# Optimization experiments

Measured on AMD Instinct MI355X. Metric: run time of the kernel, lower is better.

## Reference

```python
import jax, jax.numpy as jnp
import numpy as np

NUM_HEADS = 8
HEAD_DIM = 64
EMBED = NUM_HEADS * HEAD_DIM  # 512
KERNEL = 4
TOP_K = 8
SCALING = HEAD_DIM ** (-0.5)


def setup_inputs() -> dict:
    key = jax.random.key(0)
    ks = jax.random.split(key, 5)
    b, s = 4, 4096
    hidden_states = jax.random.normal(ks[0], (b, s, EMBED), dtype=jnp.float32)
    init = 1.0 / np.sqrt(EMBED)
    Wq = jax.random.normal(ks[1], (EMBED, EMBED), dtype=jnp.float32) * init
    Wk = jax.random.normal(ks[2], (EMBED, EMBED), dtype=jnp.float32) * init
    Wv = jax.random.normal(ks[3], (EMBED, EMBED), dtype=jnp.float32) * init
    Wo = jax.random.normal(ks[4], (EMBED, EMBED), dtype=jnp.float32) * init
    return {"hidden_states": hidden_states, "Wq": Wq, "Wk": Wk, "Wv": Wv, "Wo": Wo}


def reference(hidden_states, Wq, Wk, Wv, Wo):
    b, s, _ = hidden_states.shape
    # Q/K/V projections, split heads: (b, s, h, d)
    q = (hidden_states @ Wq).reshape(b, s, NUM_HEADS, HEAD_DIM)
    k = (hidden_states @ Wk).reshape(b, s, NUM_HEADS, HEAD_DIM)
    v = (hidden_states @ Wv).reshape(b, s, NUM_HEADS, HEAD_DIM)

    # KVCachePooling: chunk-mean along seq (s divisible by KERNEL, no pad)
    nc = s // KERNEL
    pooled_k = k.reshape(b, nc, KERNEL, NUM_HEADS, HEAD_DIM).mean(axis=2)  # (b, nc, h, d)
    pooled_v = v.reshape(b, nc, KERNEL, NUM_HEADS, HEAD_DIM).mean(axis=2)

    # TopKSparseRouter: routing scores (b, h, s, nc), reduce heads(max) then queries(max)
    qh = jnp.transpose(q, (0, 2, 1, 3))  # (b, h, s, d)
    route = jnp.einsum('bhsd,bchd->bhsc', qh, pooled_k) * SCALING
    route = route.max(axis=1).max(axis=1)  # (b, nc)
    _, top_idx = jax.lax.top_k(route, TOP_K)  # (b, k)

    # Gather selected pooled chunks: (b, k, h, d)
    k_sel = jnp.take_along_axis(pooled_k, top_idx[:, :, None, None], axis=1)
    v_sel = jnp.take_along_axis(pooled_v, top_idx[:, :, None, None], axis=1)

    # Sparse attention over the k selected chunks only
    attn = jnp.einsum('bhsd,bkhd->bhsk', qh, k_sel) * SCALING  # (b, h, s, k)
    attn = jax.nn.softmax(attn, axis=-1)
    out = jnp.einsum('bhsk,bkhd->bhsd', attn, v_sel)  # (b, h, s, d)
    out = jnp.transpose(out, (0, 2, 1, 3)).reshape(b, s, EMBED)
    return out @ Wo
```

## Files before the change

kernel.cpp:

```cpp
#include <hip/hip_runtime.h>

#define SEQ 4096
#define BATCH 4
#define EMB 512
#define NHEAD 8
#define HDIM 64
#define NCHUNK 1024
#define TOPK 8
#define NSEL 32
#define SCALING 0.125f

typedef unsigned int uint;
typedef unsigned short ushort_t;
typedef __attribute__((ext_vector_type(8))) short short8;
typedef __attribute__((ext_vector_type(4))) float f32x4;
typedef __attribute__((ext_vector_type(4))) unsigned short us4;
typedef __attribute__((ext_vector_type(8))) unsigned short us8;

__device__ __forceinline__ ushort_t bf16_rn(float x) {
  uint b = __float_as_uint(x);
  return (ushort_t)((b + 0x7FFFu + ((b >> 16) & 1u)) >> 16);
}
__device__ __forceinline__ float bf16_f(ushort_t u) {
  return __uint_as_float(((uint)u) << 16);
}

__device__ __forceinline__ void load_lds16(const void* g, void* l) {
  __builtin_amdgcn_global_load_lds(
      (const __attribute__((address_space(1))) unsigned int*)g,
      (__attribute__((address_space(3))) unsigned int*)l, 16, 0, 0);
}

__device__ __forceinline__ f32x4 mfma16(short8 a, short8 b, f32x4 c) {
  return __builtin_amdgcn_mfma_f32_16x16x32_bf16(a, b, c, 0, 0, 0);
}

__global__ __launch_bounds__(256) void wtrans_kernel(
    const float* __restrict__ Wq, const float* __restrict__ Wk,
    const float* __restrict__ Wv,
    ushort_t* __restrict__ Wtq_h, ushort_t* __restrict__ Wtq_l,
    ushort_t* __restrict__ Wtkv_h, ushort_t* __restrict__ Wtkv_l) {
  __shared__ float t[64][65];
  const int z = blockIdx.z;
  const float* src = (z == 0) ? Wq : (z == 1) ? Wk : Wv;
  ushort_t* dh = (z == 0) ? Wtq_h : Wtkv_h;
  ushort_t* dl = (z == 0) ? Wtq_l : Wtkv_l;
  const size_t obase = (z == 2) ? (size_t)512 * 512 : 0;
  const int k0 = blockIdx.x * 64, n0 = blockIdx.y * 64;
  const int tid = threadIdx.x;
#pragma unroll
  for (int i = 0; i < 4; ++i) {
    int row = (tid >> 4) + i * 16, col = (tid & 15) * 4;
    float4 v = *(const float4*)&src[(size_t)(k0 + row) * 512 + n0 + col];
    t[row][col + 0] = v.x; t[row][col + 1] = v.y;
    t[row][col + 2] = v.z; t[row][col + 3] = v.w;
  }
  __syncthreads();
#pragma unroll
  for (int i = 0; i < 4; ++i) {
    int nrow = (tid >> 4) + i * 16, kcol = (tid & 15) * 4;
    us4 h, l;
#pragma unroll
    for (int j = 0; j < 4; ++j) {
      float v = t[kcol + j][nrow];
      ushort_t hb = bf16_rn(v);
      h[j] = hb;
      l[j] = bf16_rn(v - bf16_f(hb));
    }
    size_t o = obase + (size_t)(n0 + nrow) * 512 + k0 + kcol;
    *(us4*)&dh[o] = h;
    *(us4*)&dl[o] = l;
  }
}

__global__ __launch_bounds__(256) void pool_split_kernel(
    const float* __restrict__ H, ushort_t* __restrict__ Hh,
    ushort_t* __restrict__ Hl, ushort_t* __restrict__ Hph,
    ushort_t* __restrict__ Hpl) {
  const int idx = blockIdx.x * 256 + threadIdx.x;
  const int e4 = (idx & 127) << 2;
  const int c = (idx >> 7) & 1023;
  const int b = idx >> 17;
  const size_t rbase = ((size_t)(b * SEQ + c * 4)) * 512 + e4;
  float4 s = make_float4(0.f, 0.f, 0.f, 0.f);
#pragma unroll
  for (int j = 0; j < 4; ++j) {
    float4 v = *(const float4*)&H[rbase + (size_t)j * 512];
    s.x += v.x; s.y += v.y; s.z += v.z; s.w += v.w;
    us4 h, l;
    float a[4] = {v.x, v.y, v.z, v.w};
#pragma unroll
    for (int q = 0; q < 4; ++q) {
      ushort_t hb = bf16_rn(a[q]);
      h[q] = hb;
      l[q] = bf16_rn(a[q] - bf16_f(hb));
    }
    *(us4*)&Hh[rbase + (size_t)j * 512] = h;
    *(us4*)&Hl[rbase + (size_t)j * 512] = l;
  }
  float a[4] = {s.x * 0.25f, s.y * 0.25f, s.z * 0.25f, s.w * 0.25f};
  us4 h, l;
#pragma unroll
  for (int q = 0; q < 4; ++q) {
    ushort_t hb = bf16_rn(a[q]);
    h[q] = hb;
    l[q] = bf16_rn(a[q] - bf16_f(hb));
  }
  size_t po = ((size_t)(b * NCHUNK + c)) * 512 + e4;
  *(us4*)&Hph[po] = h;
  *(us4*)&Hpl[po] = l;
}

__global__ __launch_bounds__(256) void gemm_mfma3(
    const ushort_t* __restrict__ Ah, const ushort_t* __restrict__ Al,
    const ushort_t* __restrict__ Bh, const ushort_t* __restrict__ Bl,
    ushort_t* __restrict__ Ch, ushort_t* __restrict__ Cl, int ldc) {
  __shared__ ushort_t lds[2][4][4096];
  const int tid = threadIdx.x, lane = tid & 63, wv = tid >> 6;
  const int l15 = lane & 15, g = lane >> 4;
  const int wm = wv >> 1, wn = wv & 1;
  const int row0 = blockIdx.y * 128, col0 = blockIdx.x * 128;
  const ushort_t* A0 = Ah + (size_t)row0 * 512;
  const ushort_t* B0 = Bh + (size_t)col0 * 512;
  const ushort_t* A1 = Al + (size_t)row0 * 512;
  const ushort_t* B1 = Bl + (size_t)col0 * 512;
  f32x4 acc[4][4];
#pragma unroll
  for (int m = 0; m < 4; ++m)
#pragma unroll
    for (int n = 0; n < 4; ++n) acc[m][n] = (f32x4){0.f, 0.f, 0.f, 0.f};

  auto stage = [&](int buf, int t) {
#pragma unroll
    for (int j = 0; j < 2; ++j) {
      int si = j * 256 + wv * 64 + lane;
      int row = si >> 2;
      int kb = ((si & 3) << 4) ^ (((row >> 1) & 3) << 4);
      size_t goff = (size_t)row * 512 + t * 32 + (kb >> 1);
      int doff = (j * 256 + wv * 64) * 8;
      load_lds16(A0 + goff, &lds[buf][0][doff]);
      load_lds16(B0 + goff, &lds[buf][1][doff]);
      load_lds16(A1 + goff, &lds[buf][2][doff]);
      load_lds16(B1 + goff, &lds[buf][3][doff]);
    }
  };

  stage(0, 0);
  int cur = 0;
  for (int t = 0; t < 16; ++t) {
    __syncthreads();
    if (t < 15) stage(cur ^ 1, t + 1);
    short8 ah[4], bh[4], al[4], bl[4];
#pragma unroll
    for (int m = 0; m < 4; ++m) {
      int r = wm * 64 + m * 16 + l15;
      int kb = (g << 4) ^ (((r >> 1) & 3) << 4);
      ah[m] = *(const short8*)&lds[cur][0][r * 32 + (kb >> 1)];
      al[m] = *(const short8*)&lds[cur][2][r * 32 + (kb >> 1)];
    }
#pragma unroll
    for (int n = 0; n < 4; ++n) {
      int r = wn * 64 + n * 16 + l15;
      int kb = (g << 4) ^ (((r >> 1) & 3) << 4);
      bh[n] = *(const short8*)&lds[cur][1][r * 32 + (kb >> 1)];
      bl[n] = *(const short8*)&lds[cur][3][r * 32 + (kb >> 1)];
    }
#pragma unroll
    for (int m = 0; m < 4; ++m)
#pragma unroll
      for (int n = 0; n < 4; ++n) {
        acc[m][n] = mfma16(ah[m], bh[n], acc[m][n]);
        acc[m][n] = mfma16(ah[m], bl[n], acc[m][n]);
        acc[m][n] = mfma16(al[m], bh[n], acc[m][n]);
      }
    cur ^= 1;
  }
#pragma unroll
  for (int m = 0; m < 4; ++m)
#pragma unroll
    for (int n = 0; n < 4; ++n)
#pragma unroll
      for (int q = 0; q < 4; ++q) {
        int row = row0 + wm * 64 + m * 16 + g * 4 + q;
        int col = col0 + wn * 64 + n * 16 + l15;
        float v = acc[m][n][q];
        size_t o = (size_t)row * ldc + col;
        ushort_t hb = bf16_rn(v);
        Ch[o] = hb;
        Cl[o] = bf16_rn(v - bf16_f(hb));
      }
}

__device__ __forceinline__ uint float_key(float f) {
  uint bits = __float_as_uint(f);
  return (bits & 0x80000000u) ? ~bits : (bits | 0x80000000u);
}

__device__ __forceinline__ void stage128x64(const ushort_t* src, int stride,
                                            ushort_t* dst, int wv, int lane) {
#pragma unroll
  for (int j = 0; j < 4; ++j) {
    int si = j * 256 + wv * 64 + lane;
    int row = si >> 3;
    int kb = ((si & 7) << 4) ^ ((row & 7) << 4);
    load_lds16(src + (size_t)row * stride + (kb >> 1),
               dst + (size_t)(j * 256 + wv * 64) * 8);
  }
}

template <int NPROD>
__global__ __launch_bounds__(256) void route_mfma(
    const ushort_t* __restrict__ Qh, const ushort_t* __restrict__ Ql,
    const ushort_t* __restrict__ Pkh, const ushort_t* __restrict__ Pkl,
    int kstride, int ncap, uint* __restrict__ route) {
  constexpr int NB = (NPROD == 3) ? 2 : 1;
  __shared__ ushort_t Alds[2][NB][128 * 64];
  __shared__ ushort_t Blds[NB][128 * 64];
  __shared__ float red[2][128];
  const int tid = threadIdx.x, lane = tid & 63, wv = tid >> 6;
  const int l15 = lane & 15, g = lane >> 4;
  const int wm = wv >> 1, wc = wv & 1;
  const int c0 = blockIdx.x * 128;
  const int h = blockIdx.y >> 1, sb = blockIdx.y & 1;
  const int b = blockIdx.z;
  const int s0 = sb * 2048;
  const ushort_t* Qhb = Qh + ((size_t)b * SEQ) * 512 + h * 64;
  const ushort_t* Qlb = Ql + ((size_t)b * SEQ) * 512 + h * 64;
  const ushort_t* Pkhb = Pkh + ((size_t)(b * ncap + c0)) * kstride + h * 64;
  const ushort_t* Pklb = Pkl + ((size_t)(b * ncap + c0)) * kstride + h * 64;

  stage128x64(Pkhb, kstride, &Blds[0][0], wv, lane);
  if constexpr (NPROD == 3) stage128x64(Pklb, kstride, &Blds[1][0], wv, lane);
  __syncthreads();
  short8 bh[2][4], bl[2][4];
#pragma unroll
  for (int kk = 0; kk < 2; ++kk)
#pragma unroll
    for (int n = 0; n < 4; ++n) {
      int r = wc * 64 + n * 16 + l15;
      int kb = (kk * 64 + (g << 4)) ^ ((r & 7) << 4);
      bh[kk][n] = *(const short8*)&Blds[0][r * 64 + (kb >> 1)];
      if constexpr (NPROD == 3)
        bl[kk][n] = *(const short8*)&Blds[1][r * 64 + (kb >> 1)];
    }

  float rmax[4] = {-1e30f, -1e30f, -1e30f, -1e30f};
  stage128x64(Qhb + (size_t)s0 * 512, 512, &Alds[0][0][0], wv, lane);
  if constexpr (NPROD == 3)
    stage128x64(Qlb + (size_t)s0 * 512, 512, &Alds[0][1][0], wv, lane);
  int cur = 0;
  for (int it = 0; it < 16; ++it) {
    __syncthreads();
    if (it < 15) {
      size_t so = (size_t)(s0 + (it + 1) * 128) * 512;
      stage128x64(Qhb + so, 512, &Alds[cur ^ 1][0][0], wv, lane);
      if constexpr (NPROD == 3)
        stage128x64(Qlb + so, 512, &Alds[cur ^ 1][1][0], wv, lane);
    }
    f32x4 acc[4][4];
#pragma unroll
    for (int m = 0; m < 4; ++m)
#pragma unroll
      for (int n = 0; n < 4; ++n) acc[m][n] = (f32x4){0.f, 0.f, 0.f, 0.f};
#pragma unroll
    for (int kk = 0; kk < 2; ++kk) {
      short8 ah[4], al[4];
#pragma unroll
      for (int m = 0; m < 4; ++m) {
        int r = wm * 64 + m * 16 + l15;
        int kb = (kk * 64 + (g << 4)) ^ ((r & 7) << 4);
        ah[m] = *(const short8*)&Alds[cur][0][r * 64 + (kb >> 1)];
        if constexpr (NPROD == 3)
          al[m] = *(const short8*)&Alds[cur][1][r * 64 + (kb >> 1)];
      }
#pragma unroll
      for (int m = 0; m < 4; ++m)
#pragma unroll
        for (int n = 0; n < 4; ++n) {
          acc[m][n] = mfma16(ah[m], bh[kk][n], acc[m][n]);
          if constexpr (NPROD == 3) {
            acc[m][n] = mfma16(ah[m], bl[kk][n], acc[m][n]);
            acc[m][n] = mfma16(al[m], bh[kk][n], acc[m][n]);
          }
        }
    }
#pragma unroll
    for (int n = 0; n < 4; ++n)
#pragma unroll
      for (int m = 0; m < 4; ++m)
        rmax[n] = fmaxf(rmax[n],
                        fmaxf(fmaxf(acc[m][n][0], acc[m][n][1]),
                              fmaxf(acc[m][n][2], acc[m][n][3])));
    cur ^= 1;
  }
#pragma unroll
  for (int n = 0; n < 4; ++n) {
    float v = rmax[n];
    v = fmaxf(v, __shfl_xor(v, 16, 64));
    v = fmaxf(v, __shfl_xor(v, 32, 64));
    if (g == 0) red[wm][wc * 64 + n * 16 + l15] = v;
  }
  __syncthreads();
  if (tid < 128) {
    float v = fmaxf(red[0][tid], red[1][tid]);
    atomicMax(&route[b * ncap + c0 + tid], float_key(v));
  }
}

__global__ __launch_bounds__(256) void topk_sel(const uint* __restrict__ route,
                                                int* __restrict__ cand) {
  const int b = blockIdx.x, tid = threadIdx.x;
  __shared__ unsigned long long keys[NCHUNK];
  __shared__ unsigned long long red[256];
#pragma unroll
  for (int i = 0; i < 4; ++i) {
    int idx = tid + i * 256;
    keys[idx] = ((unsigned long long)route[b * NCHUNK + idx] << 32) |
                (uint)(NCHUNK - 1 - idx);
  }
  __syncthreads();
  for (int it = 0; it < NSEL; ++it) {
    unsigned long long mx = keys[tid];
#pragma unroll
    for (int i = 1; i < 4; ++i) {
      unsigned long long k = keys[tid + i * 256];
      mx = (k > mx) ? k : mx;
    }
    red[tid] = mx;
    __syncthreads();
    for (int st = 128; st > 0; st >>= 1) {
      if (tid < st) {
        unsigned long long k = red[tid + st];
        if (k > red[tid]) red[tid] = k;
      }
      __syncthreads();
    }
    int widx = NCHUNK - 1 - (int)(red[0] & 0xffffffffu);
    if (tid == 0) {
      cand[b * NSEL + it] = widx;
      keys[widx] = 0ULL;
    }
    __syncthreads();
  }
}

__global__ __launch_bounds__(256) void gather_kernel(
    const ushort_t* __restrict__ Pkvh, const ushort_t* __restrict__ Pkvl,
    const int* __restrict__ cand, ushort_t* __restrict__ Pkch,
    ushort_t* __restrict__ Pkcl) {
  const int row = blockIdx.x, b = blockIdx.y, tid = threadIdx.x;
  size_t dst = ((size_t)(b * 128 + row)) * 512;
  if (row < NSEL) {
    int c = cand[b * NSEL + row];
    size_t src = ((size_t)(b * NCHUNK + c)) * 1024;
#pragma unroll
    for (int i = 0; i < 2; ++i) {
      Pkch[dst + tid + i * 256] = Pkvh[src + tid + i * 256];
      Pkcl[dst + tid + i * 256] = Pkvl[src + tid + i * 256];
    }
  } else {
#pragma unroll
    for (int i = 0; i < 2; ++i) {
      Pkch[dst + tid + i * 256] = 0;
      Pkcl[dst + tid + i * 256] = 0;
    }
  }
}

__global__ __launch_bounds__(64) void topk_final(const uint* __restrict__ route2,
                                                 const int* __restrict__ cand,
                                                 int* __restrict__ topidx) {
  const int b = blockIdx.x, lane = threadIdx.x;
  uint key = (lane < NSEL) ? route2[b * 128 + lane] : 0u;
  const int myc = (lane < NSEL) ? cand[b * NSEL + lane] : 0;
  for (int it = 0; it < TOPK; ++it) {
    unsigned long long kk =
        ((unsigned long long)key << 32) | (uint)(63 - lane);
#pragma unroll
    for (int o = 32; o > 0; o >>= 1) {
      unsigned long long ot = __shfl_xor(kk, o, 64);
      kk = (ot > kk) ? ot : kk;
    }
    int widx = 63 - (int)(kk & 0xffffffffu);
    if (lane == widx) {
      topidx[b * TOPK + it] = myc;
      key = 0u;
    }
  }
}

__global__ __launch_bounds__(256) void attn_p_kernel(
    const ushort_t* __restrict__ Qh, const ushort_t* __restrict__ Ql,
    const ushort_t* __restrict__ Pkvh, const ushort_t* __restrict__ Pkvl,
    const int* __restrict__ topidx, ushort_t* __restrict__ Ph,
    ushort_t* __restrict__ Pl) {
  __shared__ float Ksel[8][64];
  const int tid = threadIdx.x;
  const int st = blockIdx.x, h = blockIdx.y, b = blockIdx.z;
  if (tid < 128) {
    int j = tid >> 4, part = tid & 15;
    int c = topidx[b * TOPK + j];
    size_t base = ((size_t)(b * NCHUNK + c)) * 1024 + h * 64 + part * 4;
#pragma unroll
    for (int q = 0; q < 4; ++q)
      Ksel[j][part * 4 + q] = bf16_f(Pkvh[base + q]) + bf16_f(Pkvl[base + q]);
  }
  __syncthreads();
  const int s = st * 256 + tid;
  const size_t qbase = ((size_t)(b * SEQ + s)) * 512 + h * 64;
  float qf[64];
#pragma unroll
  for (int i = 0; i < 8; ++i) {
    us8 vh = *(const us8*)&Qh[qbase + i * 8];
    us8 vl = *(const us8*)&Ql[qbase + i * 8];
#pragma unroll
    for (int k = 0; k < 8; ++k) qf[i * 8 + k] = bf16_f(vh[k]) + bf16_f(vl[k]);
  }
  float sc[TOPK], m = -1e30f;
#pragma unroll
  for (int j = 0; j < TOPK; ++j) {
    float dot = 0.f;
#pragma unroll
    for (int d4 = 0; d4 < 16; ++d4) {
      float4 kv = *(const float4*)&Ksel[j][d4 * 4];
      dot += qf[d4 * 4 + 0] * kv.x + qf[d4 * 4 + 1] * kv.y +
             qf[d4 * 4 + 2] * kv.z + qf[d4 * 4 + 3] * kv.w;
    }
    sc[j] = dot * SCALING;
    m = fmaxf(m, sc[j]);
  }
  float se = 0.f, w8[TOPK];
#pragma unroll
  for (int j = 0; j < TOPK; ++j) {
    w8[j] = __expf(sc[j] - m);
    se += w8[j];
  }
  const float inv = 1.f / se;
  us8 ph8, pl8;
#pragma unroll
  for (int j = 0; j < TOPK; ++j) {
    float pv = w8[j] * inv;
    ushort_t hb = bf16_rn(pv);
    ph8[j] = hb;
    pl8[j] = bf16_rn(pv - bf16_f(hb));
  }
  size_t po = ((size_t)(b * SEQ + s)) * 64 + h * 8;
  *(us8*)&Ph[po] = ph8;
  *(us8*)&Pl[po] = pl8;
}

__global__ __launch_bounds__(256) void vw_kernel(
    const ushort_t* __restrict__ Pkvh, const ushort_t* __restrict__ Pkvl,
    const float* __restrict__ Wo, const int* __restrict__ topidx,
    ushort_t* __restrict__ VWth, ushort_t* __restrict__ VWtl) {
  __shared__ float Vs[8][512];
  const int tid = threadIdx.x, et = blockIdx.x, b = blockIdx.y;
#pragma unroll
  for (int i = 0; i < 16; ++i) {
    int idx = tid + i * 256;
    int j = idx >> 9, d = idx & 511;
    int c = topidx[b * TOPK + j];
    size_t src = ((size_t)(b * NCHUNK + c)) * 1024 + 512 + d;
    Vs[j][d] = bf16_f(Pkvh[src]) + bf16_f(Pkvl[src]);
  }
  __syncthreads();
  const int e = et * 64 + (tid & 63), qr = tid >> 6;
  ushort_t hbuf[16], lbuf[16];
#pragma unroll
  for (int i = 0; i < 16; ++i) {
    int hj = qr * 16 + i, h = hj >> 3, j = hj & 7;
    float dot = 0.f;
#pragma unroll
    for (int d = 0; d < 64; ++d)
      dot += Vs[j][h * 64 + d] * Wo[(size_t)(h * 64 + d) * 512 + e];
    ushort_t hb = bf16_rn(dot);
    hbuf[i] = hb;
    lbuf[i] = bf16_rn(dot - bf16_f(hb));
  }
  size_t o = ((size_t)(b * 512 + e)) * 64 + qr * 16;
  *(us8*)&VWth[o] = *(us8*)&hbuf[0];
  *(us8*)&VWth[o + 8] = *(us8*)&hbuf[8];
  *(us8*)&VWtl[o] = *(us8*)&lbuf[0];
  *(us8*)&VWtl[o + 8] = *(us8*)&lbuf[8];
}

__global__ __launch_bounds__(256) void pvw_gemm(
    const ushort_t* __restrict__ Ph, const ushort_t* __restrict__ Pl,
    const ushort_t* __restrict__ VWth, const ushort_t* __restrict__ VWtl,
    float* __restrict__ out) {
  __shared__ ushort_t lds[2][4][4096];
  const int tid = threadIdx.x, lane = tid & 63, wv = tid >> 6;
  const int l15 = lane & 15, g = lane >> 4;
  const int wm = wv >> 1, wn = wv & 1;
  const int row0 = blockIdx.y * 128, col0 = blockIdx.x * 128;
  const int b = row0 >> 12;
  const ushort_t* A0 = Ph + (size_t)row0 * 64;
  const ushort_t* A1 = Pl + (size_t)row0 * 64;
  const ushort_t* B0 = VWth + ((size_t)(b * 512 + col0)) * 64;
  const ushort_t* B1 = VWtl + ((size_t)(b * 512 + col0)) * 64;
  f32x4 acc[4][4];
#pragma unroll
  for (int m = 0; m < 4; ++m)
#pragma unroll
    for (int n = 0; n < 4; ++n) acc[m][n] = (f32x4){0.f, 0.f, 0.f, 0.f};

  auto stage = [&](int buf, int t) {
#pragma unroll
    for (int j = 0; j < 2; ++j) {
      int si = j * 256 + wv * 64 + lane;
      int row = si >> 2;
      int kb = ((si & 3) << 4) ^ (((row >> 1) & 3) << 4);
      size_t goff = (size_t)row * 64 + t * 32 + (kb >> 1);
      int doff = (j * 256 + wv * 64) * 8;
      load_lds16(A0 + goff, &lds[buf][0][doff]);
      load_lds16(B0 + goff, &lds[buf][1][doff]);
      load_lds16(A1 + goff, &lds[buf][2][doff]);
      load_lds16(B1 + goff, &lds[buf][3][doff]);
    }
  };

  stage(0, 0);
  for (int t = 0; t < 2; ++t) {
    __syncthreads();
    if (t == 0) stage(1, 1);
    short8 ah[4], bh[4], al[4], bl[4];
#pragma unroll
    for (int m = 0; m < 4; ++m) {
      int r = wm * 64 + m * 16 + l15;
      int kb = (g << 4) ^ (((r >> 1) & 3) << 4);
      ah[m] = *(const short8*)&lds[t][0][r * 32 + (kb >> 1)];
      al[m] = *(const short8*)&lds[t][2][r * 32 + (kb >> 1)];
    }
#pragma unroll
    for (int n = 0; n < 4; ++n) {
      int r = wn * 64 + n * 16 + l15;
      int kb = (g << 4) ^ (((r >> 1) & 3) << 4);
      bh[n] = *(const short8*)&lds[t][1][r * 32 + (kb >> 1)];
      bl[n] = *(const short8*)&lds[t][3][r * 32 + (kb >> 1)];
    }
#pragma unroll
    for (int m = 0; m < 4; ++m)
#pragma unroll
      for (int n = 0; n < 4; ++n) {
        acc[m][n] = mfma16(ah[m], bh[n], acc[m][n]);
        acc[m][n] = mfma16(ah[m], bl[n], acc[m][n]);
        acc[m][n] = mfma16(al[m], bh[n], acc[m][n]);
      }
  }
#pragma unroll
  for (int m = 0; m < 4; ++m)
#pragma unroll
    for (int n = 0; n < 4; ++n)
#pragma unroll
      for (int q = 0; q < 4; ++q) {
        int row = row0 + wm * 64 + m * 16 + g * 4 + q;
        int col = col0 + wn * 64 + n * 16 + l15;
        out[(size_t)row * 512 + col] = acc[m][n][q];
      }
}

extern "C" void kernel_launch(void* const* d_in, const int* in_sizes, int n_in,
                              void* d_out, int out_size, void* d_ws, size_t ws_size,
                              hipStream_t stream) {
  const float* H = (const float*)d_in[0];
  const float* Wq = (const float*)d_in[1];
  const float* Wk = (const float*)d_in[2];
  const float* Wv = (const float*)d_in[3];
  const float* Wo = (const float*)d_in[4];
  float* out = (float*)d_out;

  char* p = (char*)d_ws;
  auto alloc = [&](size_t bytes) {
    void* r = (void*)p;
    p += (bytes + 255) & ~(size_t)255;
    return r;
  };
  const size_t BS = (size_t)BATCH * SEQ;
  const size_t BC = (size_t)BATCH * NCHUNK;
  ushort_t* Hh = (ushort_t*)alloc(BS * 512 * 2);
  ushort_t* Hl = (ushort_t*)alloc(BS * 512 * 2);
  ushort_t* Hph = (ushort_t*)alloc(BC * 512 * 2);
  ushort_t* Hpl = (ushort_t*)alloc(BC * 512 * 2);
  ushort_t* Wtq_h = (ushort_t*)alloc(512 * 512 * 2);
  ushort_t* Wtq_l = (ushort_t*)alloc(512 * 512 * 2);
  ushort_t* Wtkv_h = (ushort_t*)alloc(1024 * 512 * 2);
  ushort_t* Wtkv_l = (ushort_t*)alloc(1024 * 512 * 2);
  ushort_t* Qh = (ushort_t*)alloc(BS * 512 * 2);
  ushort_t* Ql = (ushort_t*)alloc(BS * 512 * 2);
  ushort_t* Pkvh = (ushort_t*)alloc(BC * 1024 * 2);
  ushort_t* Pkvl = (ushort_t*)alloc(BC * 1024 * 2);
  ushort_t* Pkch = (ushort_t*)alloc((size_t)BATCH * 128 * 512 * 2);
  ushort_t* Pkcl = (ushort_t*)alloc((size_t)BATCH * 128 * 512 * 2);
  ushort_t* Ph = (ushort_t*)alloc(BS * 64 * 2);
  ushort_t* Pl = (ushort_t*)alloc(BS * 64 * 2);
  ushort_t* VWth = (ushort_t*)alloc((size_t)BATCH * 512 * 64 * 2);
  ushort_t* VWtl = (ushort_t*)alloc((size_t)BATCH * 512 * 64 * 2);
  uint* route = (uint*)alloc(BC * 4);
  uint* route2 = (uint*)alloc((size_t)BATCH * 128 * 4);
  int* cand = (int*)alloc(BATCH * NSEL * 4);
  int* topidx = (int*)alloc(BATCH * TOPK * 4);

  wtrans_kernel<<<dim3(8, 8, 3), 256, 0, stream>>>(
      Wq, Wk, Wv, Wtq_h, Wtq_l, Wtkv_h, Wtkv_l);
  pool_split_kernel<<<2048, 256, 0, stream>>>(H, Hh, Hl, Hph, Hpl);
  gemm_mfma3<<<dim3(4, 128), 256, 0, stream>>>(Hh, Hl, Wtq_h, Wtq_l, Qh, Ql, 512);
  gemm_mfma3<<<dim3(8, 32), 256, 0, stream>>>(Hph, Hpl, Wtkv_h, Wtkv_l, Pkvh,
                                              Pkvl, 1024);
  hipMemsetAsync(route, 0, BC * 4, stream);
  hipMemsetAsync(route2, 0, (size_t)BATCH * 128 * 4, stream);
  route_mfma<1><<<dim3(8, 16, 4), 256, 0, stream>>>(Qh, nullptr, Pkvh, nullptr,
                                                    1024, 1024, route);
  topk_sel<<<BATCH, 256, 0, stream>>>(route, cand);
  gather_kernel<<<dim3(128, BATCH), 256, 0, stream>>>(Pkvh, Pkvl, cand, Pkch,
                                                      Pkcl);
  route_mfma<3><<<dim3(1, 16, 4), 256, 0, stream>>>(Qh, Ql, Pkch, Pkcl, 512,
                                                    128, route2);
  topk_final<<<BATCH, 64, 0, stream>>>(route2, cand, topidx);
  attn_p_kernel<<<dim3(16, 8, 4), 256, 0, stream>>>(Qh, Ql, Pkvh, Pkvl, topidx,
                                                    Ph, Pl);
  vw_kernel<<<dim3(8, BATCH), 256, 0, stream>>>(Pkvh, Pkvl, Wo, topidx, VWth,
                                                VWtl);
  pvw_gemm<<<dim3(4, 128), 256, 0, stream>>>(Ph, Pl, VWth, VWtl, out);
  (void)in_sizes; (void)n_in; (void)out_size; (void)ws_size;
}
```

Measured before the change: 275.9 us.

## Merge projections, bitonic top-k, fused rescore, and fuse softmax with output GEMM

Merges the Q and pooled-KV projection GEMMs into one launch and folds the route buffer memsets into the pooling kernel. Replaces the 32-round serial argmax selection with an LDS bitonic sort. Replaces the gather-then-rescore pass with a rescore kernel that loads candidate rows directly and is spread over many more blocks. Fuses the attention softmax with the P×VW output GEMM so the P intermediate never goes to global memory. Together these cut launch count, serial selection latency and intermediate traffic, at the cost of more register pressure and lower occupancy in the fused output kernel.

Result: faster. 256.7 us (-6.9%).

```diff
diff --git a/kernel.cpp b/kernel.cpp
--- a/kernel.cpp
+++ b/kernel.cpp
@@ -33,6 +33,11 @@
 
 __device__ __forceinline__ f32x4 mfma16(short8 a, short8 b, f32x4 c) {
   return __builtin_amdgcn_mfma_f32_16x16x32_bf16(a, b, c, 0, 0, 0);
+}
+
+__device__ __forceinline__ uint float_key(float f) {
+  uint bits = __float_as_uint(f);
+  return (bits & 0x80000000u) ? ~bits : (bits | 0x80000000u);
 }
 
 __global__ __launch_bounds__(256) void wtrans_kernel(
@@ -76,8 +81,9 @@
 __global__ __launch_bounds__(256) void pool_split_kernel(
     const float* __restrict__ H, ushort_t* __restrict__ Hh,
     ushort_t* __restrict__ Hl, ushort_t* __restrict__ Hph,
-    ushort_t* __restrict__ Hpl) {
+    ushort_t* __restrict__ Hpl, uint* __restrict__ route) {
   const int idx = blockIdx.x * 256 + threadIdx.x;
+  if (idx < BATCH * NCHUNK) route[idx] = 0;
   const int e4 = (idx & 127) << 2;
   const int c = (idx >> 7) & 1023;
   const int b = idx >> 17;
@@ -111,19 +117,32 @@
   *(us4*)&Hpl[po] = l;
 }
 
-__global__ __launch_bounds__(256) void gemm_mfma3(
-    const ushort_t* __restrict__ Ah, const ushort_t* __restrict__ Al,
-    const ushort_t* __restrict__ Bh, const ushort_t* __restrict__ Bl,
-    ushort_t* __restrict__ Ch, ushort_t* __restrict__ Cl, int ldc) {
+__global__ __launch_bounds__(256) void proj_kernel(
+    const ushort_t* __restrict__ Hh, const ushort_t* __restrict__ Hl,
+    const ushort_t* __restrict__ Hph, const ushort_t* __restrict__ Hpl,
+    const ushort_t* __restrict__ Wtq_h, const ushort_t* __restrict__ Wtq_l,
+    const ushort_t* __restrict__ Wtkv_h, const ushort_t* __restrict__ Wtkv_l,
+    ushort_t* __restrict__ Qh, ushort_t* __restrict__ Ql,
+    ushort_t* __restrict__ Pkvh, ushort_t* __restrict__ Pkvl) {
   __shared__ ushort_t lds[2][4][4096];
+  const int bid = blockIdx.x;
+  const ushort_t *A0, *A1, *B0, *B1;
+  ushort_t *Ch, *Cl;
+  int ldc, row0, col0;
+  if (bid < 512) {
+    row0 = (bid >> 2) * 128; col0 = (bid & 3) * 128;
+    A0 = Hh; A1 = Hl; B0 = Wtq_h; B1 = Wtq_l; Ch = Qh; Cl = Ql; ldc = 512;
+  } else {
+    int b2 = bid - 512;
+    row0 = (b2 >> 3) * 128; col0 = (b2 & 7) * 128;
+    A0 = Hph; A1 = Hpl; B0 = Wtkv_h; B1 = Wtkv_l; Ch = Pkvh; Cl = Pkvl;
+    ldc = 1024;
+  }
+  A0 += (size_t)row0 * 512; A1 += (size_t)row0 * 512;
+  B0 += (size_t)col0 * 512; B1 += (size_t)col0 * 512;
   const int tid = threadIdx.x, lane = tid & 63, wv = tid >> 6;
   const int l15 = lane & 15, g = lane >> 4;
   const int wm = wv >> 1, wn = wv & 1;
-  const int row0 = blockIdx.y * 128, col0 = blockIdx.x * 128;
-  const ushort_t* A0 = Ah + (size_t)row0 * 512;
-  const ushort_t* B0 = Bh + (size_t)col0 * 512;
-  const ushort_t* A1 = Al + (size_t)row0 * 512;
-  const ushort_t* B1 = Bl + (size_t)col0 * 512;
   f32x4 acc[4][4];
 #pragma unroll
   for (int m = 0; m < 4; ++m)
@@ -191,11 +210,6 @@
       }
 }
 
-__device__ __forceinline__ uint float_key(float f) {
-  uint bits = __float_as_uint(f);
-  return (bits & 0x80000000u) ? ~bits : (bits | 0x80000000u);
-}
-
 __device__ __forceinline__ void stage128x64(const ushort_t* src, int stride,
                                             ushort_t* dst, int wv, int lane) {
 #pragma unroll
@@ -208,14 +222,11 @@
   }
 }
 
-template <int NPROD>
-__global__ __launch_bounds__(256) void route_mfma(
-    const ushort_t* __restrict__ Qh, const ushort_t* __restrict__ Ql,
-    const ushort_t* __restrict__ Pkh, const ushort_t* __restrict__ Pkl,
-    int kstride, int ncap, uint* __restrict__ route) {
-  constexpr int NB = (NPROD == 3) ? 2 : 1;
-  __shared__ ushort_t Alds[2][NB][128 * 64];
-  __shared__ ushort_t Blds[NB][128 * 64];
+__global__ __launch_bounds__(256) void route_screen(
+    const ushort_t* __restrict__ Qh, const ushort_t* __restrict__ Pkh,
+    uint* __restrict__ route) {
+  __shared__ ushort_t Alds[2][128 * 64];
+  __shared__ ushort_t Blds[128 * 64];
   __shared__ float red[2][128];
   const int tid = threadIdx.x, lane = tid & 63, wv = tid >> 6;
   const int l15 = lane & 15, g = lane >> 4;
@@ -225,37 +236,28 @@
   const int b = blockIdx.z;
   const int s0 = sb * 2048;
   const ushort_t* Qhb = Qh + ((size_t)b * SEQ) * 512 + h * 64;
-  const ushort_t* Qlb = Ql + ((size_t)b * SEQ) * 512 + h * 64;
-  const ushort_t* Pkhb = Pkh + ((size_t)(b * ncap + c0)) * kstride + h * 64;
-  const ushort_t* Pklb = Pkl + ((size_t)(b * ncap + c0)) * kstride + h * 64;
-
-  stage128x64(Pkhb, kstride, &Blds[0][0], wv, lane);
-  if constexpr (NPROD == 3) stage128x64(Pklb, kstride, &Blds[1][0], wv, lane);
-  __syncthreads();
-  short8 bh[2][4], bl[2][4];
+  const ushort_t* Pkhb = Pkh + ((size_t)(b * NCHUNK + c0)) * 1024 + h * 64;
+
+  stage128x64(Pkhb, 1024, &Blds[0], wv, lane);
+  __syncthreads();
+  short8 bh[2][4];
 #pragma unroll
   for (int kk = 0; kk < 2; ++kk)
 #pragma unroll
     for (int n = 0; n < 4; ++n) {
       int r = wc * 64 + n * 16 + l15;
       int kb = (kk * 64 + (g << 4)) ^ ((r & 7) << 4);
-      bh[kk][n] = *(const short8*)&Blds[0][r * 64 + (kb >> 1)];
-      if constexpr (NPROD == 3)
-        bl[kk][n] = *(const short8*)&Blds[1][r * 64 + (kb >> 1)];
+      bh[kk][n] = *(const short8*)&Blds[r * 64 + (kb >> 1)];
     }
 
   float rmax[4] = {-1e30f, -1e30f, -1e30f, -1e30f};
-  stage128x64(Qhb + (size_t)s0 * 512, 512, &Alds[0][0][0], wv, lane);
-  if constexpr (NPROD == 3)
-    stage128x64(Qlb + (size_t)s0 * 512, 512, &Alds[0][1][0], wv, lane);
+  stage128x64(Qhb + (size_t)s0 * 512, 512, &Alds[0][0], wv, lane);
   int cur = 0;
   for (int it = 0; it < 16; ++it) {
     __syncthreads();
     if (it < 15) {
       size_t so = (size_t)(s0 + (it + 1) * 128) * 512;
-      stage128x64(Qhb + so, 512, &Alds[cur ^ 1][0][0], wv, lane);
-      if constexpr (NPROD == 3)
-        stage128x64(Qlb + so, 512, &Alds[cur ^ 1][1][0], wv, lane);
+      stage128x64(Qhb + so, 512, &Alds[cur ^ 1][0], wv, lane);
     }
     f32x4 acc[4][4];
 #pragma unroll
@@ -264,25 +266,18 @@
       for (int n = 0; n < 4; ++n) acc[m][n] = (f32x4){0.f, 0.f, 0.f, 0.f};
 #pragma unroll
     for (int kk = 0; kk < 2; ++kk) {
-      short8 ah[4], al[4];
+      short8 ah[4];
 #pragma unroll
       for (int m = 0; m < 4; ++m) {
         int r = wm * 64 + m * 16 + l15;
         int kb = (kk * 64 + (g << 4)) ^ ((r & 7) << 4);
-        ah[m] = *(const short8*)&Alds[cur][0][r * 64 + (kb >> 1)];
-        if constexpr (NPROD == 3)
-          al[m] = *(const short8*)&Alds[cur][1][r * 64 + (kb >> 1)];
+        ah[m] = *(const short8*)&Alds[cur][r * 64 + (kb >> 1)];
       }
 #pragma unroll
       for (int m = 0; m < 4; ++m)
 #pragma unroll
-        for (int n = 0; n < 4; ++n) {
+        for (int n = 0; n < 4; ++n)
           acc[m][n] = mfma16(ah[m], bh[kk][n], acc[m][n]);
-          if constexpr (NPROD == 3) {
-            acc[m][n] = mfma16(ah[m], bl[kk][n], acc[m][n]);
-            acc[m][n] = mfma16(al[m], bh[kk][n], acc[m][n]);
-          }
-        }
     }
 #pragma unroll
     for (int n = 0; n < 4; ++n)
@@ -303,67 +298,115 @@
   __syncthreads();
   if (tid < 128) {
     float v = fmaxf(red[0][tid], red[1][tid]);
-    atomicMax(&route[b * ncap + c0 + tid], float_key(v));
+    atomicMax(&route[b * NCHUNK + c0 + tid], float_key(v));
   }
 }
 
 __global__ __launch_bounds__(256) void topk_sel(const uint* __restrict__ route,
-                                                int* __restrict__ cand) {
+                                                int* __restrict__ cand,
+                                                uint* __restrict__ route2) {
   const int b = blockIdx.x, tid = threadIdx.x;
   __shared__ unsigned long long keys[NCHUNK];
-  __shared__ unsigned long long red[256];
 #pragma unroll
   for (int i = 0; i < 4; ++i) {
     int idx = tid + i * 256;
     keys[idx] = ((unsigned long long)route[b * NCHUNK + idx] << 32) |
                 (uint)(NCHUNK - 1 - idx);
   }
-  __syncthreads();
-  for (int it = 0; it < NSEL; ++it) {
-    unsigned long long mx = keys[tid];
-#pragma unroll
-    for (int i = 1; i < 4; ++i) {
-      unsigned long long k = keys[tid + i * 256];
-      mx = (k > mx) ? k : mx;
-    }
-    red[tid] = mx;
-    __syncthreads();
-    for (int st = 128; st > 0; st >>= 1) {
-      if (tid < st) {
-        unsigned long long k = red[tid + st];
-        if (k > red[tid]) red[tid] = k;
+  if (tid < NSEL) route2[b * NSEL + tid] = 0;
+  __syncthreads();
+  for (int k = 2; k <= NCHUNK; k <<= 1) {
+    for (int j = k >> 1; j > 0; j >>= 1) {
+#pragma unroll
+      for (int ii = 0; ii < 4; ++ii) {
+        int i = tid + ii * 256;
+        int p = i ^ j;
+        if (p > i) {
+          bool desc = ((i & k) == 0);
+          unsigned long long a = keys[i], c = keys[p];
+          bool sw = desc ? (a < c) : (a > c);
+          if (sw) { keys[i] = c; keys[p] = a; }
+        }
       }
       __syncthreads();
     }
-    int widx = NCHUNK - 1 - (int)(red[0] & 0xffffffffu);
-    if (tid == 0) {
-      cand[b * NSEL + it] = widx;
-      keys[widx] = 0ULL;
-    }
-    __syncthreads();
-  }
-}
-
-__global__ __launch_bounds__(256) void gather_kernel(
+  }
+  if (tid < NSEL)
+    cand[b * NSEL + tid] = NCHUNK - 1 - (int)(keys[tid] & 0xffffffffu);
+}
+
+__global__ __launch_bounds__(256) void rescore_kernel(
+    const ushort_t* __restrict__ Qh, const ushort_t* __restrict__ Ql,
     const ushort_t* __restrict__ Pkvh, const ushort_t* __restrict__ Pkvl,
-    const int* __restrict__ cand, ushort_t* __restrict__ Pkch,
-    ushort_t* __restrict__ Pkcl) {
-  const int row = blockIdx.x, b = blockIdx.y, tid = threadIdx.x;
-  size_t dst = ((size_t)(b * 128 + row)) * 512;
-  if (row < NSEL) {
+    const int* __restrict__ cand, uint* __restrict__ route2) {
+  __shared__ ushort_t Ah[128 * 64], Al[128 * 64];
+  __shared__ ushort_t Bh[NSEL * 64], Bl[NSEL * 64];
+  __shared__ float red[4][NSEL];
+  const int tid = threadIdx.x, lane = tid & 63, wv = tid >> 6;
+  const int l15 = lane & 15, g = lane >> 4;
+  const int st = blockIdx.x, h = blockIdx.y, b = blockIdx.z;
+  const int s0 = st * 128;
+  {
+    int row = tid >> 3;
+    int kb = ((tid & 7) << 4) ^ ((row & 7) << 4);
     int c = cand[b * NSEL + row];
-    size_t src = ((size_t)(b * NCHUNK + c)) * 1024;
-#pragma unroll
-    for (int i = 0; i < 2; ++i) {
-      Pkch[dst + tid + i * 256] = Pkvh[src + tid + i * 256];
-      Pkcl[dst + tid + i * 256] = Pkvl[src + tid + i * 256];
-    }
-  } else {
-#pragma unroll
-    for (int i = 0; i < 2; ++i) {
-      Pkch[dst + tid + i * 256] = 0;
-      Pkcl[dst + tid + i * 256] = 0;
-    }
+    size_t src = ((size_t)(b * NCHUNK + c)) * 1024 + h * 64 + (kb >> 1);
+    load_lds16(Pkvh + src, &Bh[(size_t)(wv * 64) * 8]);
+    load_lds16(Pkvl + src, &Bl[(size_t)(wv * 64) * 8]);
+  }
+  const ushort_t* Qhb = Qh + ((size_t)(b * SEQ + s0)) * 512 + h * 64;
+  const ushort_t* Qlb = Ql + ((size_t)(b * SEQ + s0)) * 512 + h * 64;
+  stage128x64(Qhb, 512, Ah, wv, lane);
+  stage128x64(Qlb, 512, Al, wv, lane);
+  __syncthreads();
+
+  f32x4 acc[2][2];
+#pragma unroll
+  for (int m = 0; m < 2; ++m)
+#pragma unroll
+    for (int n = 0; n < 2; ++n) acc[m][n] = (f32x4){0.f, 0.f, 0.f, 0.f};
+#pragma unroll
+  for (int kk = 0; kk < 2; ++kk) {
+    short8 ah[2], al[2], bh[2], bl[2];
+#pragma unroll
+    for (int m = 0; m < 2; ++m) {
+      int r = wv * 32 + m * 16 + l15;
+      int kb = (kk * 64 + (g << 4)) ^ ((r & 7) << 4);
+      ah[m] = *(const short8*)&Ah[r * 64 + (kb >> 1)];
+      al[m] = *(const short8*)&Al[r * 64 + (kb >> 1)];
+    }
+#pragma unroll
+    for (int n = 0; n < 2; ++n) {
+      int r = n * 16 + l15;
+      int kb = (kk * 64 + (g << 4)) ^ ((r & 7) << 4);
+      bh[n] = *(const short8*)&Bh[r * 64 + (kb >> 1)];
+      bl[n] = *(const short8*)&Bl[r * 64 + (kb >> 1)];
+    }
+#pragma unroll
+    for (int m = 0; m < 2; ++m)
+#pragma unroll
+      for (int n = 0; n < 2; ++n) {
+        acc[m][n] = mfma16(ah[m], bh[n], acc[m][n]);
+        acc[m][n] = mfma16(ah[m], bl[n], acc[m][n]);
+        acc[m][n] = mfma16(al[m], bh[n], acc[m][n]);
+      }
+  }
+#pragma unroll
+  for (int n = 0; n < 2; ++n) {
+    float v = -1e30f;
+#pragma unroll
+    for (int m = 0; m < 2; ++m)
+      v = fmaxf(v, fmaxf(fmaxf(acc[m][n][0], acc[m][n][1]),
+                         fmaxf(acc[m][n][2], acc[m][n][3])));
+    v = fmaxf(v, __shfl_xor(v, 16, 64));
+    v = fmaxf(v, __shfl_xor(v, 32, 64));
+    if (g == 0) red[wv][n * 16 + l15] = v;
+  }
+  __syncthreads();
+  if (tid < NSEL) {
+    float v = fmaxf(fmaxf(red[0][tid], red[1][tid]),
+                    fmaxf(red[2][tid], red[3][tid]));
+    atomicMax(&route2[b * NSEL + tid], float_key(v));
   }
 }
 
@@ -371,11 +414,10 @@
                                                  const int* __restrict__ cand,
                                                  int* __restrict__ topidx) {
   const int b = blockIdx.x, lane = threadIdx.x;
-  uint key = (lane < NSEL) ? route2[b * 128 + lane] : 0u;
+  uint key = (lane < NSEL) ? route2[b * NSEL + lane] : 0u;
   const int myc = (lane < NSEL) ? cand[b * NSEL + lane] : 0;
   for (int it = 0; it < TOPK; ++it) {
-    unsigned long long kk =
-        ((unsigned long long)key << 32) | (uint)(63 - lane);
+    unsigned long long kk = ((unsigned long long)key << 32) | (uint)(63 - lane);
 #pragma unroll
     for (int o = 32; o > 0; o >>= 1) {
       unsigned long long ot = __shfl_xor(kk, o, 64);
@@ -387,66 +429,6 @@
       key = 0u;
     }
   }
-}
-
-__global__ __launch_bounds__(256) void attn_p_kernel(
-    const ushort_t* __restrict__ Qh, const ushort_t* __restrict__ Ql,
-    const ushort_t* __restrict__ Pkvh, const ushort_t* __restrict__ Pkvl,
-    const int* __restrict__ topidx, ushort_t* __restrict__ Ph,
-    ushort_t* __restrict__ Pl) {
-  __shared__ float Ksel[8][64];
-  const int tid = threadIdx.x;
-  const int st = blockIdx.x, h = blockIdx.y, b = blockIdx.z;
-  if (tid < 128) {
-    int j = tid >> 4, part = tid & 15;
-    int c = topidx[b * TOPK + j];
-    size_t base = ((size_t)(b * NCHUNK + c)) * 1024 + h * 64 + part * 4;
-#pragma unroll
-    for (int q = 0; q < 4; ++q)
-      Ksel[j][part * 4 + q] = bf16_f(Pkvh[base + q]) + bf16_f(Pkvl[base + q]);
-  }
-  __syncthreads();
-  const int s = st * 256 + tid;
-  const size_t qbase = ((size_t)(b * SEQ + s)) * 512 + h * 64;
-  float qf[64];
-#pragma unroll
-  for (int i = 0; i < 8; ++i) {
-    us8 vh = *(const us8*)&Qh[qbase + i * 8];
-    us8 vl = *(const us8*)&Ql[qbase + i * 8];
-#pragma unroll
-    for (int k = 0; k < 8; ++k) qf[i * 8 + k] = bf16_f(vh[k]) + bf16_f(vl[k]);
-  }
-  float sc[TOPK], m = -1e30f;
-#pragma unroll
-  for (int j = 0; j < TOPK; ++j) {
-    float dot = 0.f;
-#pragma unroll
-    for (int d4 = 0; d4 < 16; ++d4) {
-      float4 kv = *(const float4*)&Ksel[j][d4 * 4];
-      dot += qf[d4 * 4 + 0] * kv.x + qf[d4 * 4 + 1] * kv.y +
-             qf[d4 * 4 + 2] * kv.z + qf[d4 * 4 + 3] * kv.w;
-    }
-    sc[j] = dot * SCALING;
-    m = fmaxf(m, sc[j]);
-  }
-  float se = 0.f, w8[TOPK];
-#pragma unroll
-  for (int j = 0; j < TOPK; ++j) {
-    w8[j] = __expf(sc[j] - m);
-    se += w8[j];
-  }
-  const float inv = 1.f / se;
-  us8 ph8, pl8;
-#pragma unroll
-  for (int j = 0; j < TOPK; ++j) {
-    float pv = w8[j] * inv;
-    ushort_t hb = bf16_rn(pv);
-    ph8[j] = hb;
-    pl8[j] = bf16_rn(pv - bf16_f(hb));
-  }
-  size_t po = ((size_t)(b * SEQ + s)) * 64 + h * 8;
-  *(us8*)&Ph[po] = ph8;
-  *(us8*)&Pl[po] = pl8;
 }
 
 __global__ __launch_bounds__(256) void vw_kernel(
@@ -484,79 +466,130 @@
   *(us8*)&VWtl[o + 8] = *(us8*)&lbuf[8];
 }
 
-__global__ __launch_bounds__(256) void pvw_gemm(
-    const ushort_t* __restrict__ Ph, const ushort_t* __restrict__ Pl,
-    const ushort_t* __restrict__ VWth, const ushort_t* __restrict__ VWtl,
-    float* __restrict__ out) {
-  __shared__ ushort_t lds[2][4][4096];
+__global__ __launch_bounds__(256) void attn_out_kernel(
+    const ushort_t* __restrict__ Qh, const ushort_t* __restrict__ Ql,
+    const ushort_t* __restrict__ Pkvh, const ushort_t* __restrict__ Pkvl,
+    const int* __restrict__ topidx, const ushort_t* __restrict__ VWth,
+    const ushort_t* __restrict__ VWtl, float* __restrict__ out) {
+  __shared__ float Ksel[8 * 516];
+  __shared__ ushort_t Pho[64 * 64], Plo[64 * 64];
   const int tid = threadIdx.x, lane = tid & 63, wv = tid >> 6;
   const int l15 = lane & 15, g = lane >> 4;
-  const int wm = wv >> 1, wn = wv & 1;
-  const int row0 = blockIdx.y * 128, col0 = blockIdx.x * 128;
-  const int b = row0 >> 12;
-  const ushort_t* A0 = Ph + (size_t)row0 * 64;
-  const ushort_t* A1 = Pl + (size_t)row0 * 64;
-  const ushort_t* B0 = VWth + ((size_t)(b * 512 + col0)) * 64;
-  const ushort_t* B1 = VWtl + ((size_t)(b * 512 + col0)) * 64;
-  f32x4 acc[4][4];
-#pragma unroll
-  for (int m = 0; m < 4; ++m)
-#pragma unroll
-    for (int n = 0; n < 4; ++n) acc[m][n] = (f32x4){0.f, 0.f, 0.f, 0.f};
-
-  auto stage = [&](int buf, int t) {
-#pragma unroll
-    for (int j = 0; j < 2; ++j) {
-      int si = j * 256 + wv * 64 + lane;
-      int row = si >> 2;
-      int kb = ((si & 3) << 4) ^ (((row >> 1) & 3) << 4);
-      size_t goff = (size_t)row * 64 + t * 32 + (kb >> 1);
-      int doff = (j * 256 + wv * 64) * 8;
-      load_lds16(A0 + goff, &lds[buf][0][doff]);
-      load_lds16(B0 + goff, &lds[buf][1][doff]);
-      load_lds16(A1 + goff, &lds[buf][2][doff]);
-      load_lds16(B1 + goff, &lds[buf][3][doff]);
-    }
-  };
-
-  stage(0, 0);
-  for (int t = 0; t < 2; ++t) {
-    __syncthreads();
-    if (t == 0) stage(1, 1);
-    short8 ah[4], bh[4], al[4], bl[4];
-#pragma unroll
-    for (int m = 0; m < 4; ++m) {
-      int r = wm * 64 + m * 16 + l15;
-      int kb = (g << 4) ^ (((r >> 1) & 3) << 4);
-      ah[m] = *(const short8*)&lds[t][0][r * 32 + (kb >> 1)];
-      al[m] = *(const short8*)&lds[t][2][r * 32 + (kb >> 1)];
-    }
+  const int st = blockIdx.x, b = blockIdx.y;
+  const int s0 = st * 64;
+  {
+    int j = tid >> 5, h = (tid >> 2) & 7, dg = tid & 3;
+    int c = topidx[b * TOPK + j];
+    size_t base = ((size_t)(b * NCHUNK + c)) * 1024 + h * 64 + dg * 16;
+    us8 h0 = *(const us8*)&Pkvh[base], h1 = *(const us8*)&Pkvh[base + 8];
+    us8 l0 = *(const us8*)&Pkvl[base], l1 = *(const us8*)&Pkvl[base + 8];
+#pragma unroll
+    for (int ii = 0; ii < 8; ++ii) {
+      Ksel[h * 516 + j * 64 + dg * 16 + ii] = bf16_f(h0[ii]) + bf16_f(l0[ii]);
+      Ksel[h * 516 + j * 64 + dg * 16 + 8 + ii] = bf16_f(h1[ii]) + bf16_f(l1[ii]);
+    }
+  }
+  __syncthreads();
+  {
+    const int r = tid >> 2, hp = tid & 3;
+    const size_t qbase = ((size_t)(b * SEQ + s0 + r)) * 512;
+#pragma unroll
+    for (int hh = 0; hh < 2; ++hh) {
+      const int h = hp * 2 + hh;
+      float qf[64];
+#pragma unroll
+      for (int i = 0; i < 8; ++i) {
+        us8 vh = *(const us8*)&Qh[qbase + h * 64 + i * 8];
+        us8 vl = *(const us8*)&Ql[qbase + h * 64 + i * 8];
+#pragma unroll
+        for (int k2 = 0; k2 < 8; ++k2)
+          qf[i * 8 + k2] = bf16_f(vh[k2]) + bf16_f(vl[k2]);
+      }
+      float sc[TOPK], m = -1e30f;
+#pragma unroll
+      for (int j = 0; j < TOPK; ++j) {
+        float dot = 0.f;
+#pragma unroll
+        for (int d4 = 0; d4 < 16; ++d4) {
+          float4 kv = *(const float4*)&Ksel[h * 516 + j * 64 + d4 * 4];
+          dot += qf[d4 * 4 + 0] * kv.x + qf[d4 * 4 + 1] * kv.y +
+                 qf[d4 * 4 + 2] * kv.z + qf[d4 * 4 + 3] * kv.w;
+        }
+        sc[j] = dot * SCALING;
+        m = fmaxf(m, sc[j]);
+      }
+      float se = 0.f, w8[TOPK];
+#pragma unroll
+      for (int j = 0; j < TOPK; ++j) {
+        w8[j] = __expf(sc[j] - m);
+        se += w8[j];
+      }
+      const float inv = 1.f / se;
+      us8 ph8, pl8;
+#pragma unroll
+      for (int j = 0; j < TOPK; ++j) {
+        float pv = w8[j] * inv;
+        ushort_t hb = bf16_rn(pv);
+        ph8[j] = hb;
+        pl8[j] = bf16_rn(pv - bf16_f(hb));
+      }
+      int boff = (r * 128 + h * 16) ^ ((r & 7) << 4);
+      *(us8*)((char*)Pho + boff) = ph8;
+      *(us8*)((char*)Plo + boff) = pl8;
+    }
+  }
+  __syncthreads();
+  short8 pa[4][2], pb[4][2];
+#pragma unroll
+  for (int m = 0; m < 4; ++m) {
+    int r = m * 16 + l15;
+#pragma unroll
+    for (int kk = 0; kk < 2; ++kk) {
+      int boff = (r * 128 + kk * 64 + g * 16) ^ ((r & 7) << 4);
+      pa[m][kk] = *(const short8*)((const char*)Pho + boff);
+      pb[m][kk] = *(const short8*)((const char*)Plo + boff);
+    }
+  }
+#pragma unroll
+  for (int half = 0; half < 2; ++half) {
+    const int colbase = wv * 128 + half * 64;
+    short8 bh[4][2], bl[4][2];
 #pragma unroll
     for (int n = 0; n < 4; ++n) {
-      int r = wn * 64 + n * 16 + l15;
-      int kb = (g << 4) ^ (((r >> 1) & 3) << 4);
-      bh[n] = *(const short8*)&lds[t][1][r * 32 + (kb >> 1)];
-      bl[n] = *(const short8*)&lds[t][3][r * 32 + (kb >> 1)];
-    }
+      int e = colbase + n * 16 + l15;
+      size_t vb = ((size_t)(b * 512 + e)) * 64;
+#pragma unroll
+      for (int kk = 0; kk < 2; ++kk) {
+        bh[n][kk] = *(const short8*)&VWth[vb + kk * 32 + g * 8];
+        bl[n][kk] = *(const short8*)&VWtl[vb + kk * 32 + g * 8];
+      }
+    }
+    f32x4 acc[4][4];
 #pragma unroll
     for (int m = 0; m < 4; ++m)
 #pragma unroll
-      for (int n = 0; n < 4; ++n) {
-        acc[m][n] = mfma16(ah[m], bh[n], acc[m][n]);
-        acc[m][n] = mfma16(ah[m], bl[n], acc[m][n]);
-        acc[m][n] = mfma16(al[m], bh[n], acc[m][n]);
-      }
-  }
-#pragma unroll
-  for (int m = 0; m < 4; ++m)
-#pragma unroll
-    for (int n = 0; n < 4; ++n)
-#pragma unroll
-      for (int q = 0; q < 4; ++q) {
-        int row = row0 + wm * 64 + m * 16 + g * 4 + q;
-        int col = col0 + wn * 64 + n * 16 + l15;
-        out[(size_t)row * 512 + col] = acc[m][n][q];
-      }
+      for (int n = 0; n < 4; ++n) acc[m][n] = (f32x4){0.f, 0.f, 0.f, 0.f};
+#pragma unroll
+    for (int kk = 0; kk < 2; ++kk)
+#pragma unroll
+      for (int m = 0; m < 4; ++m)
+#pragma unroll
+        for (int n = 0; n < 4; ++n) {
+          acc[m][n] = mfma16(pa[m][kk], bh[n][kk], acc[m][n]);
+          acc[m][n] = mfma16(pa[m][kk], bl[n][kk], acc[m][n]);
+          acc[m][n] = mfma16(pb[m][kk], bh[n][kk], acc[m][n]);
+        }
+#pragma unroll
+    for (int m = 0; m < 4; ++m)
+#pragma unroll
+      for (int n = 0; n < 4; ++n)
+#pragma unroll
+        for (int q = 0; q < 4; ++q) {
+          int row = s0 + m * 16 + g * 4 + q;
+          int col = colbase + n * 16 + l15;
+          out[((size_t)(b * SEQ) + row) * 512 + col] = acc[m][n][q];
+        }
+  }
 }
 
 extern "C" void kernel_launch(void* const* d_in, const int* in_sizes, int n_in,
@@ -589,37 +622,26 @@
   ushort_t* Ql = (ushort_t*)alloc(BS * 512 * 2);
   ushort_t* Pkvh = (ushort_t*)alloc(BC * 1024 * 2);
   ushort_t* Pkvl = (ushort_t*)alloc(BC * 1024 * 2);
-  ushort_t* Pkch = (ushort_t*)alloc((size_t)BATCH * 128 * 512 * 2);
-  ushort_t* Pkcl = (ushort_t*)alloc((size_t)BATCH * 128 * 512 * 2);
-  ushort_t* Ph = (ushort_t*)alloc(BS * 64 * 2);
-  ushort_t* Pl = (ushort_t*)alloc(BS * 64 * 2);
   ushort_t* VWth = (ushort_t*)alloc((size_t)BATCH * 512 * 64 * 2);
   ushort_t* VWtl = (ushort_t*)alloc((size_t)BATCH * 512 * 64 * 2);
   uint* route = (uint*)alloc(BC * 4);
-  uint* route2 = (uint*)alloc((size_t)BATCH * 128 * 4);
+  uint* route2 = (uint*)alloc((size_t)BATCH * NSEL * 4);
   int* cand = (int*)alloc(BATCH * NSEL * 4);
   int* topidx = (int*)alloc(BATCH * TOPK * 4);
 
   wtrans_kernel<<<dim3(8, 8, 3), 256, 0, stream>>>(
       Wq, Wk, Wv, Wtq_h, Wtq_l, Wtkv_h, Wtkv_l);
-  pool_split_kernel<<<2048, 256, 0, stream>>>(H, Hh, Hl, Hph, Hpl);
-  gemm_mfma3<<<dim3(4, 128), 256, 0, stream>>>(Hh, Hl, Wtq_h, Wtq_l, Qh, Ql, 512);
-  gemm_mfma3<<<dim3(8, 32), 256, 0, stream>>>(Hph, Hpl, Wtkv_h, Wtkv_l, Pkvh,
-                                              Pkvl, 1024);
-  hipMemsetAsync(route, 0, BC * 4, stream);
-  hipMemsetAsync(route2, 0, (size_t)BATCH * 128 * 4, stream);
-  route_mfma<1><<<dim3(8, 16, 4), 256, 0, stream>>>(Qh, nullptr, Pkvh, nullptr,
-                                                    1024, 1024, route);
-  topk_sel<<<BATCH, 256, 0, stream>>>(route, cand);
-  gather_kernel<<<dim3(128, BATCH), 256, 0, stream>>>(Pkvh, Pkvl, cand, Pkch,
-                                                      Pkcl);
-  route_mfma<3><<<dim3(1, 16, 4), 256, 0, stream>>>(Qh, Ql, Pkch, Pkcl, 512,
-                                                    128, route2);
+  pool_split_kernel<<<2048, 256, 0, stream>>>(H, Hh, Hl, Hph, Hpl, route);
+  proj_kernel<<<768, 256, 0, stream>>>(Hh, Hl, Hph, Hpl, Wtq_h, Wtq_l,
+                                       Wtkv_h, Wtkv_l, Qh, Ql, Pkvh, Pkvl);
+  route_screen<<<dim3(8, 16, 4), 256, 0, stream>>>(Qh, Pkvh, route);
+  topk_sel<<<BATCH, 256, 0, stream>>>(route, cand, route2);
+  rescore_kernel<<<dim3(32, 8, 4), 256, 0, stream>>>(Qh, Ql, Pkvh, Pkvl, cand,
+                                                     route2);
   topk_final<<<BATCH, 64, 0, stream>>>(route2, cand, topidx);
-  attn_p_kernel<<<dim3(16, 8, 4), 256, 0, stream>>>(Qh, Ql, Pkvh, Pkvl, topidx,
-                                                    Ph, Pl);
   vw_kernel<<<dim3(8, BATCH), 256, 0, stream>>>(Pkvh, Pkvl, Wo, topidx, VWth,
                                                 VWtl);
-  pvw_gemm<<<dim3(4, 128), 256, 0, stream>>>(Ph, Pl, VWth, VWtl, out);
+  attn_out_kernel<<<dim3(64, BATCH), 256, 0, stream>>>(
+      Qh, Ql, Pkvh, Pkvl, topidx, VWth, VWtl, out);
   (void)in_sizes; (void)n_in; (void)out_size; (void)ws_size;
 }
```
